# Optimization experiments

Measured on AMD Instinct MI355X. Metric: run time of the kernel, lower is better.

The kernel has to match this reference:

```python
import jax, jax.numpy as jnp
import numpy as np

H = 2048        # hidden_size
I = 5632        # intermediate_size (SwiGLU)
E = 8           # num_experts
K = 2           # top_k
B, S = 4, 2048


def setup_inputs() -> dict:
    key = jax.random.key(0)
    ks = jax.random.split(key, 6)
    s_h = 1.0 / np.sqrt(H)
    s_i = 1.0 / np.sqrt(I)
    return {
        "hidden_states": jax.random.normal(ks[0], (B, S, H), dtype=jnp.float32),
        "Wr": jax.random.normal(ks[1], (H, E), dtype=jnp.float32) * s_h,   # router linear weight
        "br": jnp.zeros((E,), dtype=jnp.float32),                           # router bias
        "Wg": jax.random.normal(ks[2], (E, H, I), dtype=jnp.float32) * s_h, # gate_proj per expert
        "Wu": jax.random.normal(ks[3], (E, H, I), dtype=jnp.float32) * s_h, # up_proj per expert
        "Wd": jax.random.normal(ks[4], (E, I, H), dtype=jnp.float32) * s_i, # down_proj per expert
    }


def reference(hidden_states, Wr, br, Wg, Wu, Wd):
    b, s, h = hidden_states.shape
    xf = hidden_states.reshape(b * s, h)                      # [T, H]

    # Router (eval mode: no noise, no dropout)
    router_logits = xf @ Wr + br                              # [T, E]
    probs = jax.nn.softmax(router_logits, axis=-1)
    w, idx = jax.lax.top_k(probs, K)                          # [T, K]
    w = w / jnp.sum(w, axis=-1, keepdims=True)                # renormalize top-k weights

    out = jnp.zeros_like(xf)
    for e in range(E):
        # per-token combine weight for expert e (sums duplicate k-slots, as the torch loop does)
        we = jnp.sum(w * (idx == e), axis=-1)                 # [T]
        # SwiGLU expert: down(silu(gate(x)) * up(x))
        expert_out = (jax.nn.silu(xf @ Wg[e]) * (xf @ Wu[e])) @ Wd[e]  # [T, H]
        out = out + expert_out * we[:, None]
    output = out.reshape(b, s, h)
    return output, router_logits
```

## Files before the change

kernel.cpp:

```cpp
#include <hip/hip_runtime.h>

#define Hdim 2048
#define Idim 5632
#define NEXP 8
#define NTOK 8192
#define NROW 16384
#define RCAP 17408
#define MTCAP 136

#define MI_NTILES   0
#define MI_TOTAL    1
#define MI_COUNT    2
#define MI_CURSOR   10
#define MI_OFF      18
#define MI_TILEEXP  32
#define MI_ROWTOK   256
#define MI_ROWW     17664
#define MI_TOPKID   35072
#define MI_TOPKW    51456
#define META_ZERO_BYTES (35072u * 4u)

#define XG_OFF   (1ull << 19)
#define WGT_OFF  (72ull  << 20)
#define WUT_OFF  (248ull << 20)
#define HB_OFF   (424ull << 20)
#define WDT_OFF  WGT_OFF

typedef __attribute__((ext_vector_type(8))) short s8v;
typedef __attribute__((ext_vector_type(4))) float f4v;

__device__ __forceinline__ unsigned short f2bf(float f) {
  unsigned int u = __float_as_uint(f);
  u += 0x7fffu + ((u >> 16) & 1u);
  return (unsigned short)(u >> 16);
}
__device__ __forceinline__ unsigned int pack2(float lo, float hi) {
  return (__float_as_uint(lo) >> 16) | (__float_as_uint(hi) & 0xffff0000u);
}
__device__ __forceinline__ void glds16(const void* gp, void* lp) {
  __builtin_amdgcn_global_load_lds(
      (const __attribute__((address_space(1))) void*)gp,
      (__attribute__((address_space(3))) void*)lp, 16, 0, 0);
}

__global__ __launch_bounds__(256) void router_kernel(
    const float* __restrict__ x, const float* __restrict__ Wr,
    const float* __restrict__ br, float* __restrict__ logits,
    int* __restrict__ meta)
{
  int wv = threadIdx.x >> 6, lane = threadIdx.x & 63;
  int t = blockIdx.x * 4 + wv;
  const float* xr = x + (size_t)t * Hdim;
  float acc[8];
#pragma unroll
  for (int e = 0; e < 8; ++e) acc[e] = 0.f;
  for (int i = lane; i < Hdim; i += 64) {
    float xv = xr[i];
    const float4 w0 = *(const float4*)(Wr + (size_t)i * 8);
    const float4 w1 = *(const float4*)(Wr + (size_t)i * 8 + 4);
    acc[0] += xv * w0.x; acc[1] += xv * w0.y; acc[2] += xv * w0.z; acc[3] += xv * w0.w;
    acc[4] += xv * w1.x; acc[5] += xv * w1.y; acc[6] += xv * w1.z; acc[7] += xv * w1.w;
  }
#pragma unroll
  for (int off = 32; off > 0; off >>= 1)
#pragma unroll
    for (int e = 0; e < 8; ++e) acc[e] += __shfl_down(acc[e], off);
  if (lane == 0) {
    float l[8];
#pragma unroll
    for (int e = 0; e < 8; ++e) { l[e] = acc[e] + br[e]; logits[(size_t)t * 8 + e] = l[e]; }
    int i1 = 0;
#pragma unroll
    for (int e = 1; e < 8; ++e) if (l[e] > l[i1]) i1 = e;
    int i2 = -1;
#pragma unroll
    for (int e = 0; e < 8; ++e) if (e != i1 && (i2 < 0 || l[e] > l[i2])) i2 = e;
    float p2 = __expf(l[i2] - l[i1]);
    float s = 1.f + p2;
    meta[MI_TOPKID + t * 2]     = i1;
    meta[MI_TOPKID + t * 2 + 1] = i2;
    float* tw = (float*)(meta + MI_TOPKW);
    tw[t * 2] = 1.f / s; tw[t * 2 + 1] = p2 / s;
    atomicAdd(&meta[MI_COUNT + i1], 1);
    atomicAdd(&meta[MI_COUNT + i2], 1);
  }
}

__global__ void offsets_kernel(int* __restrict__ meta)
{
  __shared__ int soff[9];
  if (threadIdx.x == 0) {
    int off = 0;
#pragma unroll
    for (int e = 0; e < 8; ++e) {
      soff[e] = off;
      meta[MI_OFF + e] = off;
      meta[MI_CURSOR + e] = off;
      int c = meta[MI_COUNT + e];
      off += (c + 127) & ~127;
    }
    soff[8] = off;
    meta[MI_OFF + 8] = off;
    meta[MI_TOTAL] = off;
    meta[MI_NTILES] = off >> 7;
  }
  __syncthreads();
  int tile = threadIdx.x;
  if (tile < MTCAP) {
    int r = tile << 7;
    int e = 7;
    for (int q = 7; q >= 0; --q) if (r < soff[q + 1]) e = q;
    meta[MI_TILEEXP + tile] = e;
  }
}

__global__ __launch_bounds__(256) void scatter_kernel(int* __restrict__ meta)
{
  int idx = blockIdx.x * 256 + threadIdx.x;
  int e = meta[MI_TOPKID + idx];
  float w = ((const float*)(meta + MI_TOPKW))[idx];
  int pos = atomicAdd(&meta[MI_CURSOR + e], 1);
  meta[MI_ROWTOK + pos] = idx >> 1;
  ((float*)(meta + MI_ROWW))[pos] = w;
}

__global__ __launch_bounds__(256) void gather_kernel(
    const float* __restrict__ x, short* __restrict__ Xg,
    const int* __restrict__ meta)
{
  int r = blockIdx.x;
  int tok = meta[MI_ROWTOK + r];
  int i = threadIdx.x * 8;
  const float* src = x + (size_t)tok * Hdim + i;
  float4 a = *(const float4*)src;
  float4 b = *(const float4*)(src + 4);
  union { s8v v; unsigned short us[8]; } o;
  o.us[0] = f2bf(a.x); o.us[1] = f2bf(a.y); o.us[2] = f2bf(a.z); o.us[3] = f2bf(a.w);
  o.us[4] = f2bf(b.x); o.us[5] = f2bf(b.y); o.us[6] = f2bf(b.z); o.us[7] = f2bf(b.w);
  *(s8v*)(Xg + (size_t)r * Hdim + i) = o.v;
}

__global__ __launch_bounds__(256) void convT_kernel(
    const float* __restrict__ W, short* __restrict__ T, int K, int N)
{
  __shared__ float lds[64][65];
  int ntn = N >> 6, ntk = K >> 6;
  int per_e = ntn * ntk;
  int e = blockIdx.x / per_e;
  int r = blockIdx.x % per_e;
  int tn = r % ntn, tk = r / ntn;
  const float* We = W + (size_t)e * K * N;
  short* Te = T + (size_t)e * K * N;
  int n0 = tn << 6, k0 = tk << 6;
  int tid = threadIdx.x;
  int c = tid & 63, rr = tid >> 6;
#pragma unroll
  for (int i = 0; i < 16; ++i) {
    int k = i * 4 + rr;
    lds[c][k] = We[(size_t)(k0 + k) * N + n0 + c];
  }
  __syncthreads();
  int kp = tid & 31, nb = tid >> 5;
#pragma unroll
  for (int i = 0; i < 8; ++i) {
    int n = i * 8 + nb;
    float2 f = *(const float2*)&lds[n][kp * 2];
    unsigned int u = pack2(f.x, f.y);
    *(unsigned int*)((char*)Te + ((size_t)(n0 + n) * K + k0) * 2 + kp * 4) = u;
  }
}

__global__ __launch_bounds__(256, 2) void gateup_kernel(
    const short* __restrict__ Xg, const short* __restrict__ WgT,
    const short* __restrict__ WuT, short* __restrict__ Hbuf,
    const int* __restrict__ meta)
{
  const int NT = Idim / 128;
  int bid = blockIdx.x;
  int chunk = bid / (8 * NT);
  int rem   = bid % (8 * NT);
  int mtile = chunk * 8 + (rem & 7);
  int ntile = rem >> 3;
  if (mtile >= meta[MI_NTILES]) return;
  int e = meta[MI_TILEEXP + mtile];
  int n0 = ntile * 128;

  const short* Ab = Xg  + (size_t)(mtile * 128) * Hdim;
  const short* Gb = WgT + (size_t)e * Idim * Hdim + (size_t)n0 * Hdim;
  const short* Ub = WuT + (size_t)e * Idim * Hdim + (size_t)n0 * Hdim;

  __shared__ short sA[128 * 32];
  __shared__ short sBg[128 * 32];
  __shared__ short sBu[128 * 32];

  int tid = threadIdx.x;
  int lane = tid & 63, wv = tid >> 6;
  int wm = wv >> 1, wn = wv & 1;
  int lr = lane & 15, lg = lane >> 4;

  f4v accg[4][4], accu[4][4];
  f4v z = {0.f, 0.f, 0.f, 0.f};
#pragma unroll
  for (int a1 = 0; a1 < 4; ++a1)
#pragma unroll
    for (int b1 = 0; b1 < 4; ++b1) { accg[a1][b1] = z; accu[a1][b1] = z; }

  int e0 = tid * 8;
  int r0 = e0 >> 5, q0 = e0 & 31;
  int e1 = (256 + tid) * 8;
  int r1 = e1 >> 5, q1 = e1 & 31;
  short* d0A = &sA [(wv * 64) * 8];
  short* d1A = &sA [(256 + wv * 64) * 8];
  short* d0G = &sBg[(wv * 64) * 8];
  short* d1G = &sBg[(256 + wv * 64) * 8];
  short* d0U = &sBu[(wv * 64) * 8];
  short* d1U = &sBu[(256 + wv * 64) * 8];

  for (int kt = 0; kt < Hdim / 32; ++kt) {
    int k0 = kt * 32;
    glds16(Ab + (size_t)r0 * Hdim + k0 + q0, d0A);
    glds16(Ab + (size_t)r1 * Hdim + k0 + q1, d1A);
    glds16(Gb + (size_t)r0 * Hdim + k0 + q0, d0G);
    glds16(Gb + (size_t)r1 * Hdim + k0 + q1, d1G);
    glds16(Ub + (size_t)r0 * Hdim + k0 + q0, d0U);
    glds16(Ub + (size_t)r1 * Hdim + k0 + q1, d1U);
    __syncthreads();

    s8v a[4];
#pragma unroll
    for (int mi = 0; mi < 4; ++mi)
      a[mi] = *(const s8v*)&sA[(wm * 64 + mi * 16 + lr) * 32 + lg * 8];
#pragma unroll
    for (int ni = 0; ni < 4; ++ni) {
      int bn = wn * 64 + ni * 16 + lr;
      s8v bg = *(const s8v*)&sBg[bn * 32 + lg * 8];
      s8v bu = *(const s8v*)&sBu[bn * 32 + lg * 8];
#pragma unroll
      for (int mi = 0; mi < 4; ++mi) {
        accg[mi][ni] = __builtin_amdgcn_mfma_f32_16x16x32_bf16(a[mi], bg, accg[mi][ni], 0, 0, 0);
        accu[mi][ni] = __builtin_amdgcn_mfma_f32_16x16x32_bf16(a[mi], bu, accu[mi][ni], 0, 0, 0);
      }
    }
    __syncthreads();
  }

  int row0 = mtile * 128 + wm * 64;
#pragma unroll
  for (int mi = 0; mi < 4; ++mi) {
#pragma unroll
    for (int ni = 0; ni < 4; ++ni) {
      int col = n0 + wn * 64 + ni * 16 + lr;
#pragma unroll
      for (int r = 0; r < 4; ++r) {
        int row = row0 + mi * 16 + lg * 4 + r;
        float g = accg[mi][ni][r], u = accu[mi][ni][r];
        float h = g / (1.f + __expf(-g)) * u;
        Hbuf[(size_t)row * Idim + col] = (short)f2bf(h);
      }
    }
  }
}

__global__ __launch_bounds__(256, 2) void down_kernel(
    const short* __restrict__ Hbuf, const short* __restrict__ WdT,
    float* __restrict__ out, const int* __restrict__ meta)
{
  const int NT = Hdim / 128;
  int bid = blockIdx.x;
  int chunk = bid / (8 * NT);
  int rem   = bid % (8 * NT);
  int mtile = chunk * 8 + (rem & 7);
  int ntile = rem >> 3;
  if (mtile >= meta[MI_NTILES]) return;
  int e = meta[MI_TILEEXP + mtile];
  int n0 = ntile * 128;

  const short* Ab = Hbuf + (size_t)(mtile * 128) * Idim;
  const short* Db = WdT + (size_t)e * Hdim * Idim + (size_t)n0 * Idim;

  __shared__ short sA[128 * 32];
  __shared__ short sB[128 * 32];

  int tid = threadIdx.x;
  int lane = tid & 63, wv = tid >> 6;
  int wm = wv >> 1, wn = wv & 1;
  int lr = lane & 15, lg = lane >> 4;

  f4v acc[4][4];
  f4v z = {0.f, 0.f, 0.f, 0.f};
#pragma unroll
  for (int a1 = 0; a1 < 4; ++a1)
#pragma unroll
    for (int b1 = 0; b1 < 4; ++b1) acc[a1][b1] = z;

  int e0 = tid * 8;
  int r0 = e0 >> 5, q0 = e0 & 31;
  int e1 = (256 + tid) * 8;
  int r1 = e1 >> 5, q1 = e1 & 31;
  short* d0A = &sA[(wv * 64) * 8];
  short* d1A = &sA[(256 + wv * 64) * 8];
  short* d0B = &sB[(wv * 64) * 8];
  short* d1B = &sB[(256 + wv * 64) * 8];

  for (int kt = 0; kt < Idim / 32; ++kt) {
    int k0 = kt * 32;
    glds16(Ab + (size_t)r0 * Idim + k0 + q0, d0A);
    glds16(Ab + (size_t)r1 * Idim + k0 + q1, d1A);
    glds16(Db + (size_t)r0 * Idim + k0 + q0, d0B);
    glds16(Db + (size_t)r1 * Idim + k0 + q1, d1B);
    __syncthreads();

    s8v a[4];
#pragma unroll
    for (int mi = 0; mi < 4; ++mi)
      a[mi] = *(const s8v*)&sA[(wm * 64 + mi * 16 + lr) * 32 + lg * 8];
#pragma unroll
    for (int ni = 0; ni < 4; ++ni) {
      int bn = wn * 64 + ni * 16 + lr;
      s8v b = *(const s8v*)&sB[bn * 32 + lg * 8];
#pragma unroll
      for (int mi = 0; mi < 4; ++mi)
        acc[mi][ni] = __builtin_amdgcn_mfma_f32_16x16x32_bf16(a[mi], b, acc[mi][ni], 0, 0, 0);
    }
    __syncthreads();
  }

  int row0 = mtile * 128 + wm * 64;
  const int* rowtok = meta + MI_ROWTOK;
  const float* roww = (const float*)(meta + MI_ROWW);
#pragma unroll
  for (int mi = 0; mi < 4; ++mi) {
#pragma unroll
    for (int r = 0; r < 4; ++r) {
      int row = row0 + mi * 16 + lg * 4 + r;
      int tok = rowtok[row];
      float w = roww[row];
      float* orow = out + (size_t)tok * Hdim + n0 + wn * 64 + lr;
#pragma unroll
      for (int ni = 0; ni < 4; ++ni)
        atomicAdd(orow + ni * 16, w * acc[mi][ni][r]);
    }
  }
}

extern "C" void kernel_launch(void* const* d_in, const int* in_sizes, int n_in,
                              void* d_out, int out_size, void* d_ws, size_t ws_size,
                              hipStream_t stream)
{
  (void)in_sizes; (void)n_in; (void)out_size; (void)ws_size;
  const float* x  = (const float*)d_in[0];
  const float* Wr = (const float*)d_in[1];
  const float* br = (const float*)d_in[2];
  const float* Wg = (const float*)d_in[3];
  const float* Wu = (const float*)d_in[4];
  const float* Wd = (const float*)d_in[5];
  float* out = (float*)d_out;
  float* logits = out + (size_t)NTOK * Hdim;
  int* meta = (int*)d_ws;
  short* Xg   = (short*)((char*)d_ws + XG_OFF);
  short* WgT  = (short*)((char*)d_ws + WGT_OFF);
  short* WuT  = (short*)((char*)d_ws + WUT_OFF);
  short* WdT  = (short*)((char*)d_ws + WDT_OFF);
  short* Hbuf = (short*)((char*)d_ws + HB_OFF);

  hipMemsetAsync(d_out, 0, (size_t)NTOK * Hdim * sizeof(float), stream);
  hipMemsetAsync(d_ws, 0, META_ZERO_BYTES, stream);

  const int convBlocks = NEXP * (Idim / 64) * (Hdim / 64);

  router_kernel <<<NTOK / 4, 256, 0, stream>>>(x, Wr, br, logits, meta);
  offsets_kernel<<<1, 256, 0, stream>>>(meta);
  scatter_kernel<<<NROW / 256, 256, 0, stream>>>(meta);
  gather_kernel <<<RCAP, 256, 0, stream>>>(x, Xg, meta);
  convT_kernel  <<<convBlocks, 256, 0, stream>>>(Wg, WgT, Hdim, Idim);
  convT_kernel  <<<convBlocks, 256, 0, stream>>>(Wu, WuT, Hdim, Idim);
  gateup_kernel <<<MTCAP * (Idim / 128), 256, 0, stream>>>(Xg, WgT, WuT, Hbuf, meta);
  convT_kernel  <<<convBlocks, 256, 0, stream>>>(Wd, WdT, Idim, Hdim);
  down_kernel   <<<MTCAP * (Hdim / 128), 256, 0, stream>>>(Hbuf, WdT, out, meta);
}
```

Before: 2.174 ms.

## Restructure expert GEMMs into 256-row tiles with double-buffered swizzled LDS pipeline

Rewrites the gate/up and down grouped GEMMs to use 256-row M tiles with 512 threads, K-steps of 64, double-buffered LDS with an XOR swizzle to avoid bank conflicts, and staged async global-to-LDS loads interleaved with MFMA phases under s_setprio. Expert padding moves to 256 rows and the block index is remapped so blocks sharing an expert's weights are scheduled together. The aim is to hide load latency behind MFMA work and raise arithmetic intensity per block. In exchange it uses much more LDS per block, adds more padding rows, and relies on manual vmcnt waits and barriers that are easy to get wrong.

```diff
diff --git a/kernel.cpp b/kernel.cpp
--- a/kernel.cpp
+++ b/kernel.cpp
@@ -5,8 +5,8 @@
 #define NEXP 8
 #define NTOK 8192
 #define NROW 16384
-#define RCAP 17408
-#define MTCAP 136
+#define RCAP 18432
+#define MT256 72
 
 #define MI_NTILES   0
 #define MI_TOTAL    1
@@ -14,20 +14,23 @@
 #define MI_CURSOR   10
 #define MI_OFF      18
 #define MI_TILEEXP  32
-#define MI_ROWTOK   256
-#define MI_ROWW     17664
-#define MI_TOPKID   35072
-#define MI_TOPKW    51456
-#define META_ZERO_BYTES (35072u * 4u)
+#define MI_ROWTOK   128
+#define MI_ROWW     18560
+#define MI_TOPKID   36992
+#define MI_TOPKW    53376
+#define META_ZERO_BYTES (36992u * 4u)
 
 #define XG_OFF   (1ull << 19)
-#define WGT_OFF  (72ull  << 20)
-#define WUT_OFF  (248ull << 20)
-#define HB_OFF   (424ull << 20)
+#define WGT_OFF  (73ull  << 20)
+#define WUT_OFF  (249ull << 20)
+#define HB_OFF   (425ull << 20)
 #define WDT_OFF  WGT_OFF
 
 typedef __attribute__((ext_vector_type(8))) short s8v;
 typedef __attribute__((ext_vector_type(4))) float f4v;
+
+#define BAR()  asm volatile("s_barrier" ::: "memory")
+#define VMW2() asm volatile("s_waitcnt vmcnt(2)" ::: "memory")
 
 __device__ __forceinline__ unsigned short f2bf(float f) {
   unsigned int u = __float_as_uint(f);
@@ -37,7 +40,7 @@
 __device__ __forceinline__ unsigned int pack2(float lo, float hi) {
   return (__float_as_uint(lo) >> 16) | (__float_as_uint(hi) & 0xffff0000u);
 }
-__device__ __forceinline__ void glds16(const void* gp, void* lp) {
+__device__ __forceinline__ void glds16(const short* gp, short* lp) {
   __builtin_amdgcn_global_load_lds(
       (const __attribute__((address_space(1))) void*)gp,
       (__attribute__((address_space(3))) void*)lp, 16, 0, 0);
@@ -97,17 +100,17 @@
       meta[MI_OFF + e] = off;
       meta[MI_CURSOR + e] = off;
       int c = meta[MI_COUNT + e];
-      off += (c + 127) & ~127;
+      off += (c + 255) & ~255;
     }
     soff[8] = off;
     meta[MI_OFF + 8] = off;
     meta[MI_TOTAL] = off;
-    meta[MI_NTILES] = off >> 7;
+    meta[MI_NTILES] = off >> 8;
   }
   __syncthreads();
   int tile = threadIdx.x;
-  if (tile < MTCAP) {
-    int r = tile << 7;
+  if (tile < MT256) {
+    int r = tile << 8;
     int e = 7;
     for (int q = 7; q >= 0; --q) if (r < soff[q + 1]) e = q;
     meta[MI_TILEEXP + tile] = e;
@@ -170,90 +173,149 @@
   }
 }
 
-__global__ __launch_bounds__(256, 2) void gateup_kernel(
+
+#define ISSUE_A2(buf, h, kt) do { size_t kk_ = (size_t)(kt) * 64;                          \
+  glds16(pA + (size_t)((h) * 128      ) * strideA + kk_, &sA[(buf)][(h) * 8192 + ldst]);   \
+  glds16(pA + (size_t)((h) * 128 + 64 ) * strideA + kk_, &sA[(buf)][(h) * 8192 + 4096 + ldst]); } while (0)
+#define ISSUE_B2(arr, pB, buf, kt) do { size_t kk_ = (size_t)(kt) * 64;                    \
+  glds16((pB) + kk_,                          &arr[(buf)][ldst]);                          \
+  glds16((pB) + (size_t)64 * strideA + kk_,   &arr[(buf)][4096 + ldst]); } while (0)
+
+__global__ __launch_bounds__(512, 2) void gateup_kernel(
     const short* __restrict__ Xg, const short* __restrict__ WgT,
     const short* __restrict__ WuT, short* __restrict__ Hbuf,
     const int* __restrict__ meta)
 {
   const int NT = Idim / 128;
-  int bid = blockIdx.x;
-  int chunk = bid / (8 * NT);
-  int rem   = bid % (8 * NT);
+  int wg = (blockIdx.x & 7) * (MT256 / 8 * NT) + (blockIdx.x >> 3);
+  int chunk = wg / (8 * NT);
+  int rem   = wg % (8 * NT);
   int mtile = chunk * 8 + (rem & 7);
   int ntile = rem >> 3;
   if (mtile >= meta[MI_NTILES]) return;
   int e = meta[MI_TILEEXP + mtile];
   int n0 = ntile * 128;
-
-  const short* Ab = Xg  + (size_t)(mtile * 128) * Hdim;
-  const short* Gb = WgT + (size_t)e * Idim * Hdim + (size_t)n0 * Hdim;
-  const short* Ub = WuT + (size_t)e * Idim * Hdim + (size_t)n0 * Hdim;
-
-  __shared__ short sA[128 * 32];
-  __shared__ short sBg[128 * 32];
-  __shared__ short sBu[128 * 32];
+  const size_t strideA = Hdim;
+
+  __shared__ short sA[2][16384];
+  __shared__ short sG[2][8192];
+  __shared__ short sU[2][8192];
 
   int tid = threadIdx.x;
   int lane = tid & 63, wv = tid >> 6;
   int wm = wv >> 1, wn = wv & 1;
   int lr = lane & 15, lg = lane >> 4;
-
-  f4v accg[4][4], accu[4][4];
+  int ldst = wv * 512;
+
+  int srow = tid >> 3;
+  int kc = ((tid & 7) ^ (srow & 7)) * 8;
+  const short* pA = Xg  + (size_t)(mtile * 256) * Hdim + (size_t)srow * Hdim + kc;
+  const short* pG = WgT + (size_t)e * Idim * Hdim + (size_t)(n0 + srow) * Hdim + kc;
+  const short* pU = WuT + (size_t)e * Idim * Hdim + (size_t)(n0 + srow) * Hdim + kc;
+
+  int aoff[4][2], boff[4][2];
+#pragma unroll
+  for (int mi = 0; mi < 4; ++mi) {
+    int R = wm * 64 + mi * 16 + lr;
+#pragma unroll
+    for (int ks = 0; ks < 2; ++ks) aoff[mi][ks] = R * 64 + (((ks * 4 + lg) ^ (R & 7)) << 3);
+  }
+#pragma unroll
+  for (int ni = 0; ni < 4; ++ni) {
+    int R = wn * 64 + ni * 16 + lr;
+#pragma unroll
+    for (int ks = 0; ks < 2; ++ks) boff[ni][ks] = R * 64 + (((ks * 4 + lg) ^ (R & 7)) << 3);
+  }
+
+  f4v AG[4][4], AU[4][4];
   f4v z = {0.f, 0.f, 0.f, 0.f};
 #pragma unroll
   for (int a1 = 0; a1 < 4; ++a1)
 #pragma unroll
-    for (int b1 = 0; b1 < 4; ++b1) { accg[a1][b1] = z; accu[a1][b1] = z; }
-
-  int e0 = tid * 8;
-  int r0 = e0 >> 5, q0 = e0 & 31;
-  int e1 = (256 + tid) * 8;
-  int r1 = e1 >> 5, q1 = e1 & 31;
-  short* d0A = &sA [(wv * 64) * 8];
-  short* d1A = &sA [(256 + wv * 64) * 8];
-  short* d0G = &sBg[(wv * 64) * 8];
-  short* d1G = &sBg[(256 + wv * 64) * 8];
-  short* d0U = &sBu[(wv * 64) * 8];
-  short* d1U = &sBu[(256 + wv * 64) * 8];
-
-  for (int kt = 0; kt < Hdim / 32; ++kt) {
-    int k0 = kt * 32;
-    glds16(Ab + (size_t)r0 * Hdim + k0 + q0, d0A);
-    glds16(Ab + (size_t)r1 * Hdim + k0 + q1, d1A);
-    glds16(Gb + (size_t)r0 * Hdim + k0 + q0, d0G);
-    glds16(Gb + (size_t)r1 * Hdim + k0 + q1, d1G);
-    glds16(Ub + (size_t)r0 * Hdim + k0 + q0, d0U);
-    glds16(Ub + (size_t)r1 * Hdim + k0 + q1, d1U);
-    __syncthreads();
-
-    s8v a[4];
-#pragma unroll
-    for (int mi = 0; mi < 4; ++mi)
-      a[mi] = *(const s8v*)&sA[(wm * 64 + mi * 16 + lr) * 32 + lg * 8];
+    for (int b1 = 0; b1 < 4; ++b1) { AG[a1][b1] = z; AU[a1][b1] = z; }
+
+  const int NKT = Hdim / 64;
+
+  ISSUE_A2(0, 0, 0); ISSUE_A2(0, 1, 0);
+  ISSUE_B2(sG, pG, 0, 0); ISSUE_B2(sU, pU, 0, 0);
+  ISSUE_A2(1, 0, 1);
+  VMW2(); BAR();
+
+#define GU_HALF(CUR, T)                                                                    \
+  do {                                                                                     \
+    int nx1 = (T) + 1; if (nx1 >= NKT) nx1 -= NKT;                                         \
+    int nx2 = (T) + 2; if (nx2 >= NKT) nx2 -= NKT;                                         \
+    s8v a_[4][2], g0_[2][2], g1_[2][2], u0_[2][2], u1_[2][2];                              \
+                                                 \
+    _Pragma("unroll") for (int mi = 0; mi < 4; ++mi)                                       \
+      _Pragma("unroll") for (int ks = 0; ks < 2; ++ks)                                     \
+        a_[mi][ks] = *(const s8v*)&sA[CUR][aoff[mi][ks]];                                  \
+    _Pragma("unroll") for (int ni = 0; ni < 2; ++ni)                                       \
+      _Pragma("unroll") for (int ks = 0; ks < 2; ++ks)                                     \
+        g0_[ni][ks] = *(const s8v*)&sG[CUR][boff[ni][ks]];                                 \
+    ISSUE_A2((CUR) ^ 1, 1, nx1);                                                           \
+    BAR(); __builtin_amdgcn_s_setprio(1);                                                  \
+    _Pragma("unroll") for (int mi = 0; mi < 4; ++mi)                                       \
+      _Pragma("unroll") for (int ni = 0; ni < 2; ++ni)                                     \
+        _Pragma("unroll") for (int ks = 0; ks < 2; ++ks)                                   \
+          AG[mi][ni] = __builtin_amdgcn_mfma_f32_16x16x32_bf16(a_[mi][ks], g0_[ni][ks],    \
+                                                               AG[mi][ni], 0, 0, 0);       \
+    __builtin_amdgcn_s_setprio(0); BAR();                                                  \
+                                             \
+    _Pragma("unroll") for (int ni = 0; ni < 2; ++ni)                                       \
+      _Pragma("unroll") for (int ks = 0; ks < 2; ++ks) {                                   \
+        g1_[ni][ks] = *(const s8v*)&sG[CUR][boff[2 + ni][ks]];                             \
+        u0_[ni][ks] = *(const s8v*)&sU[CUR][boff[ni][ks]];                                 \
+      }                                                                                    \
+    ISSUE_B2(sG, pG, (CUR) ^ 1, nx1);                                                      \
+    BAR(); __builtin_amdgcn_s_setprio(1);                                                  \
+    _Pragma("unroll") for (int mi = 0; mi < 4; ++mi)                                       \
+      _Pragma("unroll") for (int ni = 0; ni < 2; ++ni)                                     \
+        _Pragma("unroll") for (int ks = 0; ks < 2; ++ks)                                   \
+          AG[mi][2 + ni] = __builtin_amdgcn_mfma_f32_16x16x32_bf16(a_[mi][ks], g1_[ni][ks],\
+                                                                   AG[mi][2 + ni], 0, 0, 0);\
+    __builtin_amdgcn_s_setprio(0); BAR();                                                  \
+                                           \
+    _Pragma("unroll") for (int ni = 0; ni < 2; ++ni)                                       \
+      _Pragma("unroll") for (int ks = 0; ks < 2; ++ks)                                     \
+        u1_[ni][ks] = *(const s8v*)&sU[CUR][boff[2 + ni][ks]];                             \
+    ISSUE_B2(sU, pU, (CUR) ^ 1, nx1);                                                      \
+    BAR(); __builtin_amdgcn_s_setprio(1);                                                  \
+    _Pragma("unroll") for (int mi = 0; mi < 4; ++mi)                                       \
+      _Pragma("unroll") for (int ni = 0; ni < 2; ++ni)                                     \
+        _Pragma("unroll") for (int ks = 0; ks < 2; ++ks)                                   \
+          AU[mi][ni] = __builtin_amdgcn_mfma_f32_16x16x32_bf16(a_[mi][ks], u0_[ni][ks],    \
+                                                               AU[mi][ni], 0, 0, 0);       \
+    __builtin_amdgcn_s_setprio(0); BAR();                                                  \
+                                         \
+    ISSUE_A2(CUR, 0, nx2);                                                                 \
+    VMW2();                                                                                \
+    BAR(); __builtin_amdgcn_s_setprio(1);                                                  \
+    _Pragma("unroll") for (int mi = 0; mi < 4; ++mi)                                       \
+      _Pragma("unroll") for (int ni = 0; ni < 2; ++ni)                                     \
+        _Pragma("unroll") for (int ks = 0; ks < 2; ++ks)                                   \
+          AU[mi][2 + ni] = __builtin_amdgcn_mfma_f32_16x16x32_bf16(a_[mi][ks], u1_[ni][ks],\
+                                                                   AU[mi][2 + ni], 0, 0, 0);\
+    __builtin_amdgcn_s_setprio(0); BAR();                                                  \
+  } while (0)
+
+  for (int t = 0; t < NKT; t += 2) {
+    GU_HALF(0, t);
+    GU_HALF(1, t + 1);
+  }
+#undef GU_HALF
+
+  int row0 = mtile * 256 + wm * 64;
+  int col0 = n0 + wn * 64;
+#pragma unroll
+  for (int mi = 0; mi < 4; ++mi) {
 #pragma unroll
     for (int ni = 0; ni < 4; ++ni) {
-      int bn = wn * 64 + ni * 16 + lr;
-      s8v bg = *(const s8v*)&sBg[bn * 32 + lg * 8];
-      s8v bu = *(const s8v*)&sBu[bn * 32 + lg * 8];
-#pragma unroll
-      for (int mi = 0; mi < 4; ++mi) {
-        accg[mi][ni] = __builtin_amdgcn_mfma_f32_16x16x32_bf16(a[mi], bg, accg[mi][ni], 0, 0, 0);
-        accu[mi][ni] = __builtin_amdgcn_mfma_f32_16x16x32_bf16(a[mi], bu, accu[mi][ni], 0, 0, 0);
-      }
-    }
-    __syncthreads();
-  }
-
-  int row0 = mtile * 128 + wm * 64;
-#pragma unroll
-  for (int mi = 0; mi < 4; ++mi) {
-#pragma unroll
-    for (int ni = 0; ni < 4; ++ni) {
-      int col = n0 + wn * 64 + ni * 16 + lr;
+      int col = col0 + ni * 16 + lr;
 #pragma unroll
       for (int r = 0; r < 4; ++r) {
         int row = row0 + mi * 16 + lg * 4 + r;
-        float g = accg[mi][ni][r], u = accu[mi][ni][r];
+        float g = AG[mi][ni][r], u = AU[mi][ni][r];
         float h = g / (1.f + __expf(-g)) * u;
         Hbuf[(size_t)row * Idim + col] = (short)f2bf(h);
       }
@@ -261,71 +323,106 @@
   }
 }
 
-__global__ __launch_bounds__(256, 2) void down_kernel(
+__global__ __launch_bounds__(512, 2) void down_kernel(
     const short* __restrict__ Hbuf, const short* __restrict__ WdT,
     float* __restrict__ out, const int* __restrict__ meta)
 {
   const int NT = Hdim / 128;
-  int bid = blockIdx.x;
-  int chunk = bid / (8 * NT);
-  int rem   = bid % (8 * NT);
+  int wg = (blockIdx.x & 7) * (MT256 / 8 * NT) + (blockIdx.x >> 3);
+  int chunk = wg / (8 * NT);
+  int rem   = wg % (8 * NT);
   int mtile = chunk * 8 + (rem & 7);
   int ntile = rem >> 3;
   if (mtile >= meta[MI_NTILES]) return;
   int e = meta[MI_TILEEXP + mtile];
   int n0 = ntile * 128;
-
-  const short* Ab = Hbuf + (size_t)(mtile * 128) * Idim;
-  const short* Db = WdT + (size_t)e * Hdim * Idim + (size_t)n0 * Idim;
-
-  __shared__ short sA[128 * 32];
-  __shared__ short sB[128 * 32];
+  const size_t strideA = Idim;
+
+  __shared__ short sA[2][16384];
+  __shared__ short sB[2][8192];
 
   int tid = threadIdx.x;
   int lane = tid & 63, wv = tid >> 6;
   int wm = wv >> 1, wn = wv & 1;
   int lr = lane & 15, lg = lane >> 4;
-
-  f4v acc[4][4];
+  int ldst = wv * 512;
+
+  int srow = tid >> 3;
+  int kc = ((tid & 7) ^ (srow & 7)) * 8;
+  const short* pA = Hbuf + (size_t)(mtile * 256) * Idim + (size_t)srow * Idim + kc;
+  const short* pB = WdT  + (size_t)e * Hdim * Idim + (size_t)(n0 + srow) * Idim + kc;
+
+  int aoff[4][2], boff[4][2];
+#pragma unroll
+  for (int mi = 0; mi < 4; ++mi) {
+    int R = wm * 64 + mi * 16 + lr;
+#pragma unroll
+    for (int ks = 0; ks < 2; ++ks) aoff[mi][ks] = R * 64 + (((ks * 4 + lg) ^ (R & 7)) << 3);
+  }
+#pragma unroll
+  for (int ni = 0; ni < 4; ++ni) {
+    int R = wn * 64 + ni * 16 + lr;
+#pragma unroll
+    for (int ks = 0; ks < 2; ++ks) boff[ni][ks] = R * 64 + (((ks * 4 + lg) ^ (R & 7)) << 3);
+  }
+
+  f4v AC[4][4];
   f4v z = {0.f, 0.f, 0.f, 0.f};
 #pragma unroll
   for (int a1 = 0; a1 < 4; ++a1)
 #pragma unroll
-    for (int b1 = 0; b1 < 4; ++b1) acc[a1][b1] = z;
-
-  int e0 = tid * 8;
-  int r0 = e0 >> 5, q0 = e0 & 31;
-  int e1 = (256 + tid) * 8;
-  int r1 = e1 >> 5, q1 = e1 & 31;
-  short* d0A = &sA[(wv * 64) * 8];
-  short* d1A = &sA[(256 + wv * 64) * 8];
-  short* d0B = &sB[(wv * 64) * 8];
-  short* d1B = &sB[(256 + wv * 64) * 8];
-
-  for (int kt = 0; kt < Idim / 32; ++kt) {
-    int k0 = kt * 32;
-    glds16(Ab + (size_t)r0 * Idim + k0 + q0, d0A);
-    glds16(Ab + (size_t)r1 * Idim + k0 + q1, d1A);
-    glds16(Db + (size_t)r0 * Idim + k0 + q0, d0B);
-    glds16(Db + (size_t)r1 * Idim + k0 + q1, d1B);
-    __syncthreads();
-
-    s8v a[4];
-#pragma unroll
-    for (int mi = 0; mi < 4; ++mi)
-      a[mi] = *(const s8v*)&sA[(wm * 64 + mi * 16 + lr) * 32 + lg * 8];
-#pragma unroll
-    for (int ni = 0; ni < 4; ++ni) {
-      int bn = wn * 64 + ni * 16 + lr;
-      s8v b = *(const s8v*)&sB[bn * 32 + lg * 8];
-#pragma unroll
-      for (int mi = 0; mi < 4; ++mi)
-        acc[mi][ni] = __builtin_amdgcn_mfma_f32_16x16x32_bf16(a[mi], b, acc[mi][ni], 0, 0, 0);
-    }
-    __syncthreads();
-  }
-
-  int row0 = mtile * 128 + wm * 64;
+    for (int b1 = 0; b1 < 4; ++b1) AC[a1][b1] = z;
+
+  const int NKT = Idim / 64;
+
+  ISSUE_A2(0, 0, 0); ISSUE_A2(0, 1, 0);
+  ISSUE_B2(sB, pB, 0, 0);
+  ISSUE_A2(1, 0, 1);
+  VMW2(); BAR();
+
+#define DN_PHASE(CUR, NI, EXTRA)                                                           \
+  do {                                                                                     \
+    EXTRA;                                                                                 \
+    BAR(); __builtin_amdgcn_s_setprio(1);                                                  \
+    _Pragma("unroll") for (int mi = 0; mi < 4; ++mi)                                       \
+      _Pragma("unroll") for (int ks = 0; ks < 2; ++ks)                                     \
+        AC[mi][NI] = __builtin_amdgcn_mfma_f32_16x16x32_bf16(a_[mi][ks], b_[NI][ks],       \
+                                                             AC[mi][NI], 0, 0, 0);         \
+    __builtin_amdgcn_s_setprio(0); BAR();                                                  \
+  } while (0)
+
+#define DN_HALF(CUR, T)                                                                    \
+  do {                                                                                     \
+    int nx1 = (T) + 1; if (nx1 >= NKT) nx1 -= NKT;                                         \
+    int nx2 = (T) + 2; if (nx2 >= NKT) nx2 -= NKT;                                         \
+    s8v a_[4][2], b_[4][2];                                                                \
+                                                                \
+    _Pragma("unroll") for (int mi = 0; mi < 4; ++mi)                                       \
+      _Pragma("unroll") for (int ks = 0; ks < 2; ++ks)                                     \
+        a_[mi][ks] = *(const s8v*)&sA[CUR][aoff[mi][ks]];                                  \
+    _Pragma("unroll") for (int ni = 0; ni < 2; ++ni)                                       \
+      _Pragma("unroll") for (int ks = 0; ks < 2; ++ks)                                     \
+        b_[ni][ks] = *(const s8v*)&sB[CUR][boff[ni][ks]];                                  \
+    DN_PHASE(CUR, 0, ISSUE_A2((CUR) ^ 1, 1, nx1));                                         \
+                                                                    \
+    DN_PHASE(CUR, 1, {                                                                     \
+      _Pragma("unroll") for (int ni = 2; ni < 4; ++ni)                                     \
+        _Pragma("unroll") for (int ks = 0; ks < 2; ++ks)                                   \
+          b_[ni][ks] = *(const s8v*)&sB[CUR][boff[ni][ks]];                                \
+      ISSUE_B2(sB, pB, (CUR) ^ 1, nx1); });                                                \
+    DN_PHASE(CUR, 2, {});                                                                  \
+    DN_PHASE(CUR, 3, { ISSUE_A2(CUR, 0, nx2); VMW2(); });                                  \
+  } while (0)
+
+  for (int t = 0; t < NKT; t += 2) {
+    DN_HALF(0, t);
+    DN_HALF(1, t + 1);
+  }
+#undef DN_HALF
+#undef DN_PHASE
+
+  int row0 = mtile * 256 + wm * 64;
+  int col0 = n0 + wn * 64;
   const int* rowtok = meta + MI_ROWTOK;
   const float* roww = (const float*)(meta + MI_ROWW);
 #pragma unroll
@@ -335,10 +432,10 @@
       int row = row0 + mi * 16 + lg * 4 + r;
       int tok = rowtok[row];
       float w = roww[row];
-      float* orow = out + (size_t)tok * Hdim + n0 + wn * 64 + lr;
+      float* orow = out + (size_t)tok * Hdim + col0 + lr;
 #pragma unroll
       for (int ni = 0; ni < 4; ++ni)
-        atomicAdd(orow + ni * 16, w * acc[mi][ni][r]);
+        atomicAdd(orow + ni * 16, w * AC[mi][ni][r]);
     }
   }
 }
@@ -374,7 +471,7 @@
   gather_kernel <<<RCAP, 256, 0, stream>>>(x, Xg, meta);
   convT_kernel  <<<convBlocks, 256, 0, stream>>>(Wg, WgT, Hdim, Idim);
   convT_kernel  <<<convBlocks, 256, 0, stream>>>(Wu, WuT, Hdim, Idim);
-  gateup_kernel <<<MTCAP * (Idim / 128), 256, 0, stream>>>(Xg, WgT, WuT, Hbuf, meta);
+  gateup_kernel <<<MT256 * (Idim / 128), 512, 0, stream>>>(Xg, WgT, WuT, Hbuf, meta);
   convT_kernel  <<<convBlocks, 256, 0, stream>>>(Wd, WdT, Idim, Hdim);
-  down_kernel   <<<MTCAP * (Hdim / 128), 256, 0, stream>>>(Hbuf, WdT, out, meta);
-}
+  down_kernel   <<<MT256 * (Hdim / 128), 512, 0, stream>>>(Hbuf, WdT, out, meta);
+}
```

Measured after the change: 2.298 ms. 1.06x slower.
